# Kernel optimization log

Measured on AMD Instinct MI355X. Metric: run time of the kernel, lower is better.

Reference implementation:

```python
import jax, jax.numpy as jnp
import numpy as np

B, N, E, H, TOP_K = 2, 2048, 1024, 16, 64
Dh = E // H


def _linear_init(k, fan_in, shape):
    bound = 1.0 / np.sqrt(fan_in)
    return jax.random.uniform(k, shape, jnp.float32, -bound, bound)


def setup_inputs() -> dict:
    key = jax.random.key(0)
    ks = jax.random.split(key, 11)
    return {
        "query": jax.random.normal(ks[0], (B, N, E), jnp.float32),
        "key": jax.random.normal(ks[1], (B, N, E), jnp.float32),
        "value": jax.random.normal(ks[2], (B, N, E), jnp.float32),
        "Wq": _linear_init(ks[3], E, (E, E)),
        "bq": _linear_init(ks[4], E, (E,)),
        "Wk": _linear_init(ks[5], E, (E, E)),
        "bk": _linear_init(ks[6], E, (E,)),
        "Wv": _linear_init(ks[7], E, (E, E)),
        "bv": _linear_init(ks[8], E, (E,)),
        "Wo": _linear_init(ks[9], E, (E, E)),
        "bo": _linear_init(ks[10], E, (E,)),
    }


def _split_heads(x):
    # (B, N, E) -> (B*H, N, Dh)
    return x.reshape(B, N, H, Dh).transpose(0, 2, 1, 3).reshape(B * H, N, Dh)


def _merge_heads(x):
    # (B*H, N, Dh) -> (B, N, E)
    return x.reshape(B, H, N, Dh).transpose(0, 2, 1, 3).reshape(B, N, E)


def _topk_attention(q, k, v, top_k):
    # q,k,v: (BH, N, Dh). Faithful to _classical_efficient_attention:
    # scores scaled by sqrt(last dim of Q) == sqrt(Dh).
    scores = jnp.einsum("bqd,bkd->bqk", q, k) / jnp.sqrt(jnp.float32(q.shape[-1]))
    top_scores, top_idx = jax.lax.top_k(scores, min(top_k, scores.shape[-1]))
    w = jax.nn.softmax(top_scores, axis=-1)  # (BH, Nq, K)
    # gather V rows: (BH, 1, Nk, Dh) indexed along axis 2 -> (BH, Nq, K, Dh)
    vals = jnp.take_along_axis(v[:, None, :, :], top_idx[..., None], axis=2)
    return jnp.einsum("bqk,bqkd->bqd", w, vals)


def reference(query, key, value, Wq, bq, Wk, bk, Wv, bv, Wo, bo):
    q = _split_heads(query @ Wq.T + bq)
    k = _split_heads(key @ Wk.T + bk)
    v = _split_heads(value @ Wv.T + bv)
    out = _topk_attention(q, k, v, TOP_K)
    return _merge_heads(out) @ Wo.T + bo
```

## Files before the change

kernel.cpp:

```cpp
#include <hip/hip_runtime.h>
#include <stdint.h>
#include <math.h>

#define Bk 2
#define Nk 2048
#define Ek 1024
#define Hk 16
#define DHk 64
#define BLENDW 5e-5
#define PRECAND 96
#define CANDCAP 128

using short8 = __attribute__((ext_vector_type(8))) short;
using f32x4  = __attribute__((ext_vector_type(4))) float;

__device__ __forceinline__ unsigned short bf16rne(float f) {
    const unsigned u = __float_as_uint(f);
    return (unsigned short)((u + 0x7FFFu + ((u >> 16) & 1u)) >> 16);
}

__global__ __launch_bounds__(256) void cvt_split(
    const float* __restrict__ in, unsigned short* __restrict__ oh,
    unsigned short* __restrict__ ol)
{
    const int i = blockIdx.x * 256 + threadIdx.x;
    const float4 a = ((const float4*)in)[i * 2];
    const float4 b = ((const float4*)in)[i * 2 + 1];
    float x[8] = {a.x, a.y, a.z, a.w, b.x, b.y, b.z, b.w};
    unsigned short hs[8], ls[8];
#pragma unroll
    for (int j = 0; j < 8; ++j) {
        hs[j] = bf16rne(x[j]);
        const float hf = __uint_as_float((unsigned)hs[j] << 16);
        ls[j] = bf16rne(x[j] - hf);
    }
    uint4 ho, lo;
    ho.x = hs[0] | ((unsigned)hs[1] << 16); ho.y = hs[2] | ((unsigned)hs[3] << 16);
    ho.z = hs[4] | ((unsigned)hs[5] << 16); ho.w = hs[6] | ((unsigned)hs[7] << 16);
    lo.x = ls[0] | ((unsigned)ls[1] << 16); lo.y = ls[2] | ((unsigned)ls[3] << 16);
    lo.z = ls[4] | ((unsigned)ls[5] << 16); lo.w = ls[6] | ((unsigned)ls[7] << 16);
    ((uint4*)oh)[i] = ho;
    ((uint4*)ol)[i] = lo;
}

template<int MODE>
__global__ __launch_bounds__(256, 4) void gemm_mfma(
    const unsigned short* __restrict__ Xh, const unsigned short* __restrict__ Xl,
    const unsigned short* __restrict__ Wh, const unsigned short* __restrict__ Wl,
    const float* __restrict__ bias, float* __restrict__ out,
    unsigned short* __restrict__ obf)
{
    __shared__ unsigned short Ah[128][40], Al[128][40];
    __shared__ unsigned short Bh[64][40],  Bl[64][40];

    const int tid  = threadIdx.x;
    const int lane = tid & 63;
    const int wv   = tid >> 6;
    const int n16  = lane & 15;
    const int quad = lane >> 4;
    const int mBase = blockIdx.y * 128;
    const int nBase = blockIdx.x * 64;

    f32x4 acc[2][4];
#pragma unroll
    for (int i = 0; i < 2; ++i)
#pragma unroll
        for (int j = 0; j < 4; ++j) acc[i][j] = (f32x4){0.f, 0.f, 0.f, 0.f};

    const int arow = tid >> 1, aoff = (tid & 1) * 16;
    const int brow = tid >> 2, boff = (tid & 3) * 8;
    const size_t aIdx = (size_t)(mBase + arow) * Ek + aoff;
    const size_t bIdx = (size_t)(nBase + brow) * Ek + boff;

    for (int kt = 0; kt < Ek; kt += 32) {
        const uint4 ah0 = *(const uint4*)(Xh + aIdx + kt);
        const uint4 ah1 = *(const uint4*)(Xh + aIdx + kt + 8);
        const uint4 al0 = *(const uint4*)(Xl + aIdx + kt);
        const uint4 al1 = *(const uint4*)(Xl + aIdx + kt + 8);
        const uint4 bh0 = *(const uint4*)(Wh + bIdx + kt);
        const uint4 bl0 = *(const uint4*)(Wl + bIdx + kt);
        __syncthreads();
        *(uint4*)&Ah[arow][aoff]     = ah0;
        *(uint4*)&Ah[arow][aoff + 8] = ah1;
        *(uint4*)&Al[arow][aoff]     = al0;
        *(uint4*)&Al[arow][aoff + 8] = al1;
        *(uint4*)&Bh[brow][boff]     = bh0;
        *(uint4*)&Bl[brow][boff]     = bl0;
        __syncthreads();

        const short8 fa_h0 = *(const short8*)&Ah[wv*32 +      n16][quad*8];
        const short8 fa_l0 = *(const short8*)&Al[wv*32 +      n16][quad*8];
        const short8 fa_h1 = *(const short8*)&Ah[wv*32 + 16 + n16][quad*8];
        const short8 fa_l1 = *(const short8*)&Al[wv*32 + 16 + n16][quad*8];
#pragma unroll
        for (int ct = 0; ct < 4; ++ct) {
            const short8 fb_h = *(const short8*)&Bh[ct*16 + n16][quad*8];
            const short8 fb_l = *(const short8*)&Bl[ct*16 + n16][quad*8];
            acc[0][ct] = __builtin_amdgcn_mfma_f32_16x16x32_bf16(fa_h0, fb_h, acc[0][ct], 0, 0, 0);
            acc[0][ct] = __builtin_amdgcn_mfma_f32_16x16x32_bf16(fa_h0, fb_l, acc[0][ct], 0, 0, 0);
            acc[0][ct] = __builtin_amdgcn_mfma_f32_16x16x32_bf16(fa_l0, fb_h, acc[0][ct], 0, 0, 0);
            acc[1][ct] = __builtin_amdgcn_mfma_f32_16x16x32_bf16(fa_h1, fb_h, acc[1][ct], 0, 0, 0);
            acc[1][ct] = __builtin_amdgcn_mfma_f32_16x16x32_bf16(fa_h1, fb_l, acc[1][ct], 0, 0, 0);
            acc[1][ct] = __builtin_amdgcn_mfma_f32_16x16x32_bf16(fa_l1, fb_h, acc[1][ct], 0, 0, 0);
        }
    }

#pragma unroll
    for (int mt = 0; mt < 2; ++mt)
#pragma unroll
    for (int ct = 0; ct < 4; ++ct) {
        const int c  = nBase + ct*16 + n16;
        const float bv = bias[c];
#pragma unroll
        for (int reg = 0; reg < 4; ++reg) {
            const int m = mBase + wv*32 + mt*16 + quad*4 + reg;
            const float o = acc[mt][ct][reg] + bv;
            size_t dst;
            if (MODE == 0) {
                dst = (size_t)m * Ek + c;
            } else {
                const int bb = m >> 11, nn = m & 2047;
                const int hh = c >> 6,  dd = c & 63;
                dst = (((size_t)(bb*Hk + hh) * Nk) + nn) * DHk + dd;
            }
            out[dst] = o;
            if (MODE == 1 && obf) obf[dst] = bf16rne(o);
        }
    }
}

__device__ __forceinline__ unsigned fkey(float s) {
    const unsigned b = __float_as_uint(s);
    return (b & 0x80000000u) ? ~b : (b | 0x80000000u);
}
__device__ __forceinline__ unsigned long long dkey(double s) {
    unsigned long long b = (unsigned long long)__double_as_longlong(s);
    return (b & 0x8000000000000000ull) ? ~b : (b | 0x8000000000000000ull);
}
__device__ __forceinline__ double dinv(unsigned long long u) {
    const unsigned long long b =
        (u & 0x8000000000000000ull) ? (u & 0x7fffffffffffffffull) : ~u;
    return __longlong_as_double((long long)b);
}
__device__ __forceinline__ unsigned wave_umin(unsigned v) {
#pragma unroll
    for (int off = 32; off > 0; off >>= 1) {
        const unsigned o = (unsigned)__shfl_xor((int)v, off);
        v = v < o ? v : o;
    }
    return v;
}
__device__ __forceinline__ unsigned wave_umax(unsigned v) {
#pragma unroll
    for (int off = 32; off > 0; off >>= 1) {
        const unsigned o = (unsigned)__shfl_xor((int)v, off);
        v = v > o ? v : o;
    }
    return v;
}
__device__ __forceinline__ int wave_sum_i(int v) {
#pragma unroll
    for (int off = 32; off > 0; off >>= 1) v += __shfl_xor(v, off);
    return v;
}

__device__ __forceinline__ void proc_row(
    const int lane, const int lrow,
    unsigned s0, unsigned s1, unsigned s2, unsigned s3,
    unsigned s4, unsigned s5, unsigned s6, unsigned s7,
    unsigned s8, unsigned s9, unsigned s10, unsigned s11,
    unsigned s12, unsigned s13, unsigned s14, unsigned s15,
    const float* __restrict__ Kb, const float (*qsf)[68],
    unsigned long long (*ck)[CANDCAP], unsigned (*ci)[CANDCAP],
    unsigned (*sel_idx)[64], float (*sel_val)[64], unsigned (*eq_idx)[64],
    int& i65_out, float& lam_out)
{
    const unsigned long long lmask = (1ull << lane) - 1ull;

    const unsigned q0 = s0 << 16,  q1 = s1 << 16,  q2 = s2 << 16,  q3 = s3 << 16;
    const unsigned q4 = s4 << 16,  q5 = s5 << 16,  q6 = s6 << 16,  q7 = s7 << 16;
    const unsigned q8 = s8 << 16,  q9 = s9 << 16,  q10 = s10 << 16, q11 = s11 << 16;
    const unsigned q12 = s12 << 16, q13 = s13 << 16, q14 = s14 << 16, q15 = s15 << 16;

    unsigned m1 = 0u, m2 = 0u;
#define T2(V) { const unsigned t_ = (V) < m1 ? (V) : m1; \
                m1 = m1 > (V) ? m1 : (V);  m2 = m2 > t_ ? m2 : t_; }
    T2(s0)  T2(s1)  T2(s2)  T2(s3)  T2(s4)  T2(s5)  T2(s6)  T2(s7)
    T2(s8)  T2(s9)  T2(s10) T2(s11) T2(s12) T2(s13) T2(s14) T2(s15)
    T2(q0)  T2(q1)  T2(q2)  T2(q3)  T2(q4)  T2(q5)  T2(q6)  T2(q7)
    T2(q8)  T2(q9)  T2(q10) T2(q11) T2(q12) T2(q13) T2(q14) T2(q15)
#undef T2
    unsigned lo16 = wave_umin(m2) >> 16;
    unsigned hi16 = wave_umax(m1) >> 16;

    while (lo16 < hi16) {
        const unsigned mid = lo16 + ((hi16 - lo16) >> 1) + 1u;
        const unsigned M = mid << 16;
        int c0 = 0, c1 = 0, c2 = 0, c3 = 0;
        c0 += (s0  >= M); c0 += (q0  >= M); c0 += (s1  >= M); c0 += (q1  >= M);
        c0 += (s2  >= M); c0 += (q2  >= M); c0 += (s3  >= M); c0 += (q3  >= M);
        c1 += (s4  >= M); c1 += (q4  >= M); c1 += (s5  >= M); c1 += (q5  >= M);
        c1 += (s6  >= M); c1 += (q6  >= M); c1 += (s7  >= M); c1 += (q7  >= M);
        c2 += (s8  >= M); c2 += (q8  >= M); c2 += (s9  >= M); c2 += (q9  >= M);
        c2 += (s10 >= M); c2 += (q10 >= M); c2 += (s11 >= M); c2 += (q11 >= M);
        c3 += (s12 >= M); c3 += (q12 >= M); c3 += (s13 >= M); c3 += (q13 >= M);
        c3 += (s14 >= M); c3 += (q14 >= M); c3 += (s15 >= M); c3 += (q15 >= M);
        int c = wave_sum_i((c0 + c1) + (c2 + c3));
        c = __builtin_amdgcn_readfirstlane(c);
        if (c >= PRECAND) {
            lo16 = mid;
            if (c <= CANDCAP) break;
        } else hi16 = mid - 1u;
    }
    const unsigned THsh = lo16 << 16;

    int nc = 0;
#define COLH(IDX, PRED) { \
        const bool g = (PRED); \
        const unsigned long long m = __ballot(g); \
        if (g) { \
            const int pos = nc + __popcll(m & lmask); \
            if (pos < CANDCAP) \
                ci[lrow][pos] = (unsigned)((((IDX) >> 3) * 512) + (((IDX) & 7) * 64) + lane); \
        } \
        nc += __popcll(m); }
#define COLW(W, S, Q) COLH(2*(W), (Q) >= THsh) COLH(2*(W)+1, (S) >= THsh)
    COLW(0, s0, q0)    COLW(1, s1, q1)    COLW(2, s2, q2)    COLW(3, s3, q3)
    COLW(4, s4, q4)    COLW(5, s5, q5)    COLW(6, s6, q6)    COLW(7, s7, q7)
    COLW(8, s8, q8)    COLW(9, s9, q9)    COLW(10, s10, q10) COLW(11, s11, q11)
    COLW(12, s12, q12) COLW(13, s13, q13) COLW(14, s14, q14) COLW(15, s15, q15)
#undef COLW
#undef COLH
    if (nc > CANDCAP) nc = CANDCAP;

    const int c8 = lane >> 3, d8 = lane & 7;
    const float* qrow = &qsf[lrow][d8 * 8];
    const double qd0 = (double)qrow[0], qd1 = (double)qrow[1];
    const double qd2 = (double)qrow[2], qd3 = (double)qrow[3];
    const double qd4 = (double)qrow[4], qd5 = (double)qrow[5];
    const double qd6 = (double)qrow[6], qd7 = (double)qrow[7];
    const int nb = (nc + 7) >> 3;
    for (int b = 0; b < nb; ++b) {
        const int s  = b * 8 + c8;
        const int s2 = s < nc ? s : nc - 1;
        const unsigned cidx = ci[lrow][s2];
        const unsigned kb32 = (cidx << 6) + (unsigned)(d8 * 8);
        const float2 kv0 = *(const float2*)(Kb + kb32);
        const float2 kv1 = *(const float2*)(Kb + kb32 + 2);
        const float2 kv2 = *(const float2*)(Kb + kb32 + 4);
        const float2 kv3 = *(const float2*)(Kb + kb32 + 6);
        double acc = 0.0;
        acc = fma(qd0, (double)kv0.x, acc);
        acc = fma(qd1, (double)kv0.y, acc);
        acc = fma(qd2, (double)kv1.x, acc);
        acc = fma(qd3, (double)kv1.y, acc);
        acc = fma(qd4, (double)kv2.x, acc);
        acc = fma(qd5, (double)kv2.y, acc);
        acc = fma(qd6, (double)kv3.x, acc);
        acc = fma(qd7, (double)kv3.y, acc);
        acc += __shfl_xor(acc, 1);
        acc += __shfl_xor(acc, 2);
        acc += __shfl_xor(acc, 4);
        if (d8 == 0 && s < nc) ck[lrow][s] = dkey(acc * 0.125);
    }

    const unsigned long long k0 = (lane      < nc) ? ck[lrow][lane]      : 0ull;
    const unsigned long long k1 = (lane + 64 < nc) ? ck[lrow][lane + 64] : 0ull;
    const unsigned idx0 = ci[lrow][lane];
    const unsigned idx1 = ci[lrow][(lane + 64) & (CANDCAP - 1)];
    const unsigned kh0 = (unsigned)(k0 >> 32), kh1 = (unsigned)(k1 >> 32);
    const unsigned kl0 = (unsigned)k0,         kl1 = (unsigned)k1;

    unsigned H;
    {
        const unsigned i0 = (k0 != 0ull) ? kh0 : 0xFFFFFFFFu;
        const unsigned i1 = (k1 != 0ull) ? kh1 : 0xFFFFFFFFu;
        unsigned lo = wave_umin(i0 < i1 ? i0 : i1);
        unsigned hi = wave_umax(kh0 > kh1 ? kh0 : kh1);
        bool done = false;
        while (lo < hi) {
            const unsigned mid = lo + ((hi - lo) >> 1) + 1u;
            const int c = __popcll(__ballot(kh0 >= mid))
                        + __popcll(__ballot(kh1 >= mid));
            if (c == 64) {
                const unsigned v0 = (kh0 >= mid) ? kh0 : 0xFFFFFFFFu;
                const unsigned v1 = (kh1 >= mid) ? kh1 : 0xFFFFFFFFu;
                H = wave_umin(v0 < v1 ? v0 : v1);
                done = true; break;
            }
            if (c >= 64) lo = mid; else hi = mid - 1u;
        }
        if (!done) H = lo;
    }
    const int cGtHi = __popcll(__ballot(kh0 > H))
                    + __popcll(__ballot(kh1 > H));
    const int need1 = 64 - cGtHi;

    const bool e0v = (kh0 == H) && (k0 != 0ull);
    const bool e1v = (kh1 == H) && (k1 != 0ull);
    const int cEq = __popcll(__ballot(e0v)) + __popcll(__ballot(e1v));
    unsigned Tlo;
    if (need1 == cEq) {
        const unsigned v0 = e0v ? kl0 : 0xFFFFFFFFu;
        const unsigned v1 = e1v ? kl1 : 0xFFFFFFFFu;
        Tlo = wave_umin(v0 < v1 ? v0 : v1);
    } else if (need1 == 1) {
        const unsigned v0 = e0v ? kl0 : 0u;
        const unsigned v1 = e1v ? kl1 : 0u;
        Tlo = wave_umax(v0 > v1 ? v0 : v1);
    } else {
        unsigned lo = 0u, hi = 0xFFFFFFFFu;
        bool done = false;
        while (lo < hi) {
            const unsigned mid = lo + ((hi - lo) >> 1) + 1u;
            const int c = __popcll(__ballot(e0v && kl0 >= mid))
                        + __popcll(__ballot(e1v && kl1 >= mid));
            if (c == need1) {
                const unsigned v0 = (e0v && kl0 >= mid) ? kl0 : 0xFFFFFFFFu;
                const unsigned v1 = (e1v && kl1 >= mid) ? kl1 : 0xFFFFFFFFu;
                Tlo = wave_umin(v0 < v1 ? v0 : v1);
                done = true; break;
            }
            if (c >= need1) lo = mid; else hi = mid - 1u;
        }
        if (!done) Tlo = lo;
    }
    const unsigned long long T = ((unsigned long long)H << 32) | Tlo;

    int base = 0;
    {
        const bool g0 = k0 > T;
        unsigned long long m = __ballot(g0);
        if (g0) {
            const int pos = base + __popcll(m & lmask);
            sel_idx[lrow][pos] = idx0; sel_val[lrow][pos] = (float)dinv(k0);
        }
        base += __popcll(m);
        const bool g1 = k1 > T;
        m = __ballot(g1);
        if (g1) {
            const int pos = base + __popcll(m & lmask);
            sel_idx[lrow][pos] = idx1; sel_val[lrow][pos] = (float)dinv(k1);
        }
        base += __popcll(m);
    }

    int ne = 0;
    {
        const bool e0 = k0 == T;
        unsigned long long m = __ballot(e0);
        if (e0) {
            const int pos = ne + __popcll(m & lmask);
            if (pos < 64) eq_idx[lrow][pos] = idx0;
        }
        ne += __popcll(m);
        const bool e1 = k1 == T;
        m = __ballot(e1);
        if (e1) {
            const int pos = ne + __popcll(m & lmask);
            if (pos < 64) eq_idx[lrow][pos] = idx1;
        }
        ne += __popcll(m);
    }
    if (ne > 64) ne = 64;

    const int   need = 64 - base;
    const float tvf  = (float)dinv(T);
    if (lane < need) {
        unsigned my = 0u;
        for (int j = 0; j < ne; ++j) {
            const unsigned v = eq_idx[lrow][j];
            int rank = 0;
            for (int j2 = 0; j2 < ne; ++j2) rank += (eq_idx[lrow][j2] < v) ? 1 : 0;
            if (rank == lane) my = v;
        }
        sel_idx[lrow][base + lane] = my;
        sel_val[lrow][base + lane] = tvf;
    }

    unsigned long long m2k = 0ull;
    if (k0 < T && k0 > m2k) m2k = k0;
    if (k1 < T && k1 > m2k) m2k = k1;
#pragma unroll
    for (int off = 32; off > 0; off >>= 1) {
        const unsigned long long o =
            (unsigned long long)__shfl_xor((long long)m2k, off);
        if (o > m2k) m2k = o;
    }
    int i65 = 0;
    {
        unsigned long long mm = __ballot(k0 == m2k && m2k != 0ull);
        if (mm) i65 = __shfl((int)idx0, (int)(__ffsll((long long)mm) - 1));
        else {
            mm = __ballot(k1 == m2k && m2k != 0ull);
            if (mm) i65 = __shfl((int)idx1, (int)(__ffsll((long long)mm) - 1));
        }
    }
    double fr = (dinv(T) - dinv(m2k)) * (1.0 / BLENDW);
    if (fr > 1.0) fr = 1.0;
    i65_out = i65;
    lam_out = (m2k == 0ull) ? 0.f : (float)(0.5 * (1.0 - fr));
}

__global__ __launch_bounds__(1024, 8) void attn_topk_mfma(
    const float* __restrict__ qf, const float* __restrict__ kf,
    const unsigned short* __restrict__ kbf,
    const float* __restrict__ vh, float* __restrict__ outm)
{
    __shared__ __align__(16) char uS[33024];
    float (*sc)[516] = (float(*)[516])uS;
    unsigned long long (*ck)[CANDCAP] = (unsigned long long(*)[CANDCAP])uS;
    unsigned (*ci)[CANDCAP] = (unsigned(*)[CANDCAP])(uS + 16384);

    __shared__ float          qsf[16][68];
    __shared__ unsigned short qbf[16][72];
    __shared__ unsigned sel_idx[16][64];
    __shared__ float    sel_val[16][64];
    __shared__ unsigned eq_idx[16][64];

    const int tid  = threadIdx.x;
    const int lane = tid & 63;
    const int wv   = tid >> 6;

    const int wid  = (blockIdx.x & 7) * 512 + (blockIdx.x >> 3);
    const int slot = wid >> 7;
    const int qt   = wid & 127;
    const int bb   = slot >> 4;
    const int hh   = slot & 15;

    const float*          Qb = qf  + (size_t)slot * Nk * DHk + (size_t)qt * 16 * DHk;
    const float*          Kb = kf  + (size_t)slot * Nk * DHk;
    const unsigned short* KB = kbf + (size_t)slot * Nk * DHk;
    const float*          Vb = vh  + (size_t)slot * Nk * DHk;

    {
        const int r = tid >> 6, d = tid & 63;
        const float qv = Qb[r * DHk + d];
        qsf[r][d] = qv;
        qbf[r][d] = bf16rne(qv);
    }
    __syncthreads();

    const int n16  = lane & 15;
    const int quad = lane >> 4;
    short8 afrag0, afrag1;
    afrag0 = *(const short8*)&qbf[n16][quad * 8];
    afrag1 = *(const short8*)&qbf[n16][32 + quad * 8];

    unsigned p0, p1, p2, p3, p4, p5, p6, p7;
    unsigned p8, p9, p10, p11, p12, p13, p14, p15;
    const int rowD = quad * 4;

#define QK_TILE(CH, T, ACC) { \
    const unsigned short* kp = KB + ((size_t)(CH) * 512 + (wv * 2 + (T)) * 16 + n16) * DHk + quad * 8; \
    const short8 b0_ = *(const short8*)(kp); \
    const short8 b1_ = *(const short8*)(kp + 32); \
    ACC = __builtin_amdgcn_mfma_f32_16x16x32_bf16(afrag0, b0_, ACC, 0, 0, 0); \
    ACC = __builtin_amdgcn_mfma_f32_16x16x32_bf16(afrag1, b1_, ACC, 0, 0, 0); \
}
#define SC_STORE(T, ACC) { \
    const int ccol = (wv * 2 + (T)) * 16 + n16; \
    sc[rowD + 0][ccol] = ACC[0]; sc[rowD + 1][ccol] = ACC[1]; \
    sc[rowD + 2][ccol] = ACC[2]; sc[rowD + 3][ccol] = ACC[3]; \
}
#define PACKW(J, DEST) { \
    const unsigned lo_ = fkey(sc[wv][(2*(J)    ) * 64 + lane]) >> 16; \
    const unsigned hi_ = fkey(sc[wv][(2*(J) + 1) * 64 + lane]) >> 16; \
    DEST = lo_ | (hi_ << 16); \
}
#define DO_CHUNK(CH, D0, D1, D2, D3) { \
    f32x4 ac0 = {0.f,0.f,0.f,0.f}, ac1 = {0.f,0.f,0.f,0.f}; \
    QK_TILE(CH, 0, ac0) QK_TILE(CH, 1, ac1) \
    __syncthreads();                    \
    SC_STORE(0, ac0) SC_STORE(1, ac1) \
    __syncthreads(); \
    PACKW(0, D0) PACKW(1, D1) PACKW(2, D2) PACKW(3, D3) \
}
    DO_CHUNK(0, p0,  p1,  p2,  p3)
    DO_CHUNK(1, p4,  p5,  p6,  p7)
    DO_CHUNK(2, p8,  p9,  p10, p11)
    DO_CHUNK(3, p12, p13, p14, p15)
#undef DO_CHUNK
#undef PACKW
#undef SC_STORE
#undef QK_TILE

    __syncthreads();

    int i65_0; float lam_0;
    proc_row(lane, wv,
             p0, p1, p2, p3, p4, p5, p6, p7,
             p8, p9, p10, p11, p12, p13, p14, p15,
             Kb, qsf, ck, ci, sel_idx, sel_val, eq_idx, i65_0, lam_0);

    {
        const float    sv = sel_val[wv][lane];
        const unsigned vi = sel_idx[wv][lane];
        float mx = sv;
#pragma unroll
        for (int off = 32; off > 0; off >>= 1)
            mx = fmaxf(mx, __shfl_xor(mx, off));
        float p = __expf(sv - mx);
        float Z = p;
#pragma unroll
        for (int off = 32; off > 0; off >>= 1)
            Z += __shfl_xor(Z, off);
        const float w = p / Z;

        float acc = 0.f;
#pragma unroll 8
        for (int j = 0; j < 64; ++j) {
            const float wj = __shfl(w, j);
            const int   ij = __shfl((int)vi, j);
            const unsigned voff = ((unsigned)ij << 6) + (unsigned)lane;
            acc = fmaf(wj, Vb[voff], acc);
        }
        {
            const float wT  = __shfl(w, 63);
            const int   i64 = __shfl((int)vi, 63);
            const unsigned o65 = ((unsigned)i65_0 << 6) + (unsigned)lane;
            const unsigned o64 = ((unsigned)i64   << 6) + (unsigned)lane;
            acc += wT * lam_0 * (Vb[o65] - Vb[o64]);
        }
        const int gq = qt * 16 + wv;
        outm[((size_t)bb * Nk + gq) * Ek + hh * DHk + lane] = acc;
    }
}

extern "C" void kernel_launch(void* const* d_in, const int* in_sizes, int n_in,
                              void* d_out, int out_size, void* d_ws, size_t ws_size,
                              hipStream_t stream)
{
    const float* query = (const float*)d_in[0];
    const float* key   = (const float*)d_in[1];
    const float* value = (const float*)d_in[2];
    const float* Wq    = (const float*)d_in[3];
    const float* bq    = (const float*)d_in[4];
    const float* Wk    = (const float*)d_in[5];
    const float* bk    = (const float*)d_in[6];
    const float* Wv    = (const float*)d_in[7];
    const float* bv    = (const float*)d_in[8];
    const float* Wo    = (const float*)d_in[9];
    const float* bo    = (const float*)d_in[10];
    float* out = (float*)d_out;
    (void)in_sizes; (void)n_in; (void)out_size; (void)ws_size;

    const size_t seg  = (size_t)(Bk * Hk) * Nk * DHk;
    const size_t wseg = (size_t)Ek * Ek;
    float* qfp = (float*)d_ws;
    float* kfp = qfp + seg;
    float* vws = kfp + seg;
    float* aws = vws + seg;
    unsigned short* kbf = (unsigned short*)(aws + seg);
    unsigned short* xh  = kbf + seg;
    unsigned short* xl  = xh + seg;
    unsigned short* wh  = xl + seg;
    unsigned short* wl  = wh + wseg;

    const dim3 blk(256);
    const dim3 gG(16, 32);
    const int  gX = (int)(seg  / 2048);
    const int  gW = (int)(wseg / 2048);

    hipLaunchKernelGGL(cvt_split, dim3(gX), blk, 0, stream, query, xh, xl);
    hipLaunchKernelGGL(cvt_split, dim3(gW), blk, 0, stream, Wq, wh, wl);
    hipLaunchKernelGGL((gemm_mfma<1>), gG, blk, 0, stream, xh, xl, wh, wl, bq, qfp, (unsigned short*)nullptr);
    hipLaunchKernelGGL(cvt_split, dim3(gX), blk, 0, stream, key, xh, xl);
    hipLaunchKernelGGL(cvt_split, dim3(gW), blk, 0, stream, Wk, wh, wl);
    hipLaunchKernelGGL((gemm_mfma<1>), gG, blk, 0, stream, xh, xl, wh, wl, bk, kfp, kbf);
    hipLaunchKernelGGL(cvt_split, dim3(gX), blk, 0, stream, value, xh, xl);
    hipLaunchKernelGGL(cvt_split, dim3(gW), blk, 0, stream, Wv, wh, wl);
    hipLaunchKernelGGL((gemm_mfma<1>), gG, blk, 0, stream, xh, xl, wh, wl, bv, vws, (unsigned short*)nullptr);
    hipLaunchKernelGGL(attn_topk_mfma, dim3(32 * 128), dim3(1024), 0, stream,
                       qfp, kfp, kbf, vws, aws);
    hipLaunchKernelGGL(cvt_split, dim3(gX), blk, 0, stream, aws, xh, xl);
    hipLaunchKernelGGL(cvt_split, dim3(gW), blk, 0, stream, Wo, wh, wl);
    hipLaunchKernelGGL((gemm_mfma<0>), gG, blk, 0, stream, xh, xl, wh, wl, bo, out, (unsigned short*)nullptr);
}
```

Before: 645.7 us.

## Use 512-thread GEMM tiles, DPP wave reductions, and packed LDS weight/index pairs

```diff
diff --git a/kernel.cpp b/kernel.cpp
--- a/kernel.cpp
+++ b/kernel.cpp
@@ -44,7 +44,7 @@
 }
 
 template<int MODE>
-__global__ __launch_bounds__(256, 4) void gemm_mfma(
+__global__ __launch_bounds__(512, 4) void gemm_mfma(
     const unsigned short* __restrict__ Xh, const unsigned short* __restrict__ Xl,
     const unsigned short* __restrict__ Wh, const unsigned short* __restrict__ Wl,
     const float* __restrict__ bias, float* __restrict__ out,
@@ -61,60 +61,47 @@
     const int mBase = blockIdx.y * 128;
     const int nBase = blockIdx.x * 64;
 
-    f32x4 acc[2][4];
-#pragma unroll
-    for (int i = 0; i < 2; ++i)
-#pragma unroll
-        for (int j = 0; j < 4; ++j) acc[i][j] = (f32x4){0.f, 0.f, 0.f, 0.f};
-
-    const int arow = tid >> 1, aoff = (tid & 1) * 16;
-    const int brow = tid >> 2, boff = (tid & 3) * 8;
+    f32x4 acc[4];
+#pragma unroll
+    for (int j = 0; j < 4; ++j) acc[j] = (f32x4){0.f, 0.f, 0.f, 0.f};
+
+    const int arow = tid >> 2, aoff = (tid & 3) * 8;
+    const int brow = tid >> 3, boff = (tid & 7) * 4;
     const size_t aIdx = (size_t)(mBase + arow) * Ek + aoff;
     const size_t bIdx = (size_t)(nBase + brow) * Ek + boff;
 
     for (int kt = 0; kt < Ek; kt += 32) {
         const uint4 ah0 = *(const uint4*)(Xh + aIdx + kt);
-        const uint4 ah1 = *(const uint4*)(Xh + aIdx + kt + 8);
         const uint4 al0 = *(const uint4*)(Xl + aIdx + kt);
-        const uint4 al1 = *(const uint4*)(Xl + aIdx + kt + 8);
-        const uint4 bh0 = *(const uint4*)(Wh + bIdx + kt);
-        const uint4 bl0 = *(const uint4*)(Wl + bIdx + kt);
+        const uint2 bh0 = *(const uint2*)(Wh + bIdx + kt);
+        const uint2 bl0 = *(const uint2*)(Wl + bIdx + kt);
         __syncthreads();
-        *(uint4*)&Ah[arow][aoff]     = ah0;
-        *(uint4*)&Ah[arow][aoff + 8] = ah1;
-        *(uint4*)&Al[arow][aoff]     = al0;
-        *(uint4*)&Al[arow][aoff + 8] = al1;
-        *(uint4*)&Bh[brow][boff]     = bh0;
-        *(uint4*)&Bl[brow][boff]     = bl0;
+        *(uint4*)&Ah[arow][aoff] = ah0;
+        *(uint4*)&Al[arow][aoff] = al0;
+        *(uint2*)&Bh[brow][boff] = bh0;
+        *(uint2*)&Bl[brow][boff] = bl0;
         __syncthreads();
 
-        const short8 fa_h0 = *(const short8*)&Ah[wv*32 +      n16][quad*8];
-        const short8 fa_l0 = *(const short8*)&Al[wv*32 +      n16][quad*8];
-        const short8 fa_h1 = *(const short8*)&Ah[wv*32 + 16 + n16][quad*8];
-        const short8 fa_l1 = *(const short8*)&Al[wv*32 + 16 + n16][quad*8];
+        const short8 fa_h = *(const short8*)&Ah[wv*16 + n16][quad*8];
+        const short8 fa_l = *(const short8*)&Al[wv*16 + n16][quad*8];
 #pragma unroll
         for (int ct = 0; ct < 4; ++ct) {
             const short8 fb_h = *(const short8*)&Bh[ct*16 + n16][quad*8];
             const short8 fb_l = *(const short8*)&Bl[ct*16 + n16][quad*8];
-            acc[0][ct] = __builtin_amdgcn_mfma_f32_16x16x32_bf16(fa_h0, fb_h, acc[0][ct], 0, 0, 0);
-            acc[0][ct] = __builtin_amdgcn_mfma_f32_16x16x32_bf16(fa_h0, fb_l, acc[0][ct], 0, 0, 0);
-            acc[0][ct] = __builtin_amdgcn_mfma_f32_16x16x32_bf16(fa_l0, fb_h, acc[0][ct], 0, 0, 0);
-            acc[1][ct] = __builtin_amdgcn_mfma_f32_16x16x32_bf16(fa_h1, fb_h, acc[1][ct], 0, 0, 0);
-            acc[1][ct] = __builtin_amdgcn_mfma_f32_16x16x32_bf16(fa_h1, fb_l, acc[1][ct], 0, 0, 0);
-            acc[1][ct] = __builtin_amdgcn_mfma_f32_16x16x32_bf16(fa_l1, fb_h, acc[1][ct], 0, 0, 0);
-        }
-    }
-
-#pragma unroll
-    for (int mt = 0; mt < 2; ++mt)
+            acc[ct] = __builtin_amdgcn_mfma_f32_16x16x32_bf16(fa_h, fb_h, acc[ct], 0, 0, 0);
+            acc[ct] = __builtin_amdgcn_mfma_f32_16x16x32_bf16(fa_h, fb_l, acc[ct], 0, 0, 0);
+            acc[ct] = __builtin_amdgcn_mfma_f32_16x16x32_bf16(fa_l, fb_h, acc[ct], 0, 0, 0);
+        }
+    }
+
 #pragma unroll
     for (int ct = 0; ct < 4; ++ct) {
         const int c  = nBase + ct*16 + n16;
         const float bv = bias[c];
 #pragma unroll
         for (int reg = 0; reg < 4; ++reg) {
-            const int m = mBase + wv*32 + mt*16 + quad*4 + reg;
-            const float o = acc[mt][ct][reg] + bv;
+            const int m = mBase + wv*16 + quad*4 + reg;
+            const float o = acc[ct][reg] + bv;
             size_t dst;
             if (MODE == 0) {
                 dst = (size_t)m * Ek + c;
@@ -142,26 +129,40 @@
         (u & 0x8000000000000000ull) ? (u & 0x7fffffffffffffffull) : ~u;
     return __longlong_as_double((long long)b);
 }
-__device__ __forceinline__ unsigned wave_umin(unsigned v) {
-#pragma unroll
-    for (int off = 32; off > 0; off >>= 1) {
-        const unsigned o = (unsigned)__shfl_xor((int)v, off);
-        v = v < o ? v : o;
-    }
-    return v;
-}
-__device__ __forceinline__ unsigned wave_umax(unsigned v) {
-#pragma unroll
-    for (int off = 32; off > 0; off >>= 1) {
-        const unsigned o = (unsigned)__shfl_xor((int)v, off);
-        v = v > o ? v : o;
-    }
-    return v;
-}
-__device__ __forceinline__ int wave_sum_i(int v) {
-#pragma unroll
-    for (int off = 32; off > 0; off >>= 1) v += __shfl_xor(v, off);
-    return v;
+
+__device__ __forceinline__ int dpp_wsum_i32(int x) {
+#define STEP(C) x += __builtin_amdgcn_update_dpp(0, x, C, 0xf, 0xf, true);
+    STEP(0x111) STEP(0x112) STEP(0x114) STEP(0x118) STEP(0x142) STEP(0x143)
+#undef STEP
+    return __builtin_amdgcn_readlane(x, 63);
+}
+__device__ __forceinline__ float dpp_wsum_f32(float x) {
+#define STEP(C) { const int t_ = __builtin_amdgcn_update_dpp(0, __float_as_int(x), C, 0xf, 0xf, true); \
+                  x += __int_as_float(t_); }
+    STEP(0x111) STEP(0x112) STEP(0x114) STEP(0x118) STEP(0x142) STEP(0x143)
+#undef STEP
+    return __int_as_float(__builtin_amdgcn_readlane(__float_as_int(x), 63));
+}
+__device__ __forceinline__ float dpp_wmax_f32(float x) {
+#define STEP(C) { const int t_ = __builtin_amdgcn_update_dpp(__float_as_int(x), __float_as_int(x), C, 0xf, 0xf, false); \
+                  x = fmaxf(x, __int_as_float(t_)); }
+    STEP(0x111) STEP(0x112) STEP(0x114) STEP(0x118) STEP(0x142) STEP(0x143)
+#undef STEP
+    return __int_as_float(__builtin_amdgcn_readlane(__float_as_int(x), 63));
+}
+__device__ __forceinline__ unsigned dpp_wmin_u32(unsigned x) {
+#define STEP(C) { const unsigned t_ = (unsigned)__builtin_amdgcn_update_dpp((int)x, (int)x, C, 0xf, 0xf, false); \
+                  x = x < t_ ? x : t_; }
+    STEP(0x111) STEP(0x112) STEP(0x114) STEP(0x118) STEP(0x142) STEP(0x143)
+#undef STEP
+    return (unsigned)__builtin_amdgcn_readlane((int)x, 63);
+}
+__device__ __forceinline__ unsigned dpp_wmax_u32(unsigned x) {
+#define STEP(C) { const unsigned t_ = (unsigned)__builtin_amdgcn_update_dpp((int)x, (int)x, C, 0xf, 0xf, false); \
+                  x = x > t_ ? x : t_; }
+    STEP(0x111) STEP(0x112) STEP(0x114) STEP(0x118) STEP(0x142) STEP(0x143)
+#undef STEP
+    return (unsigned)__builtin_amdgcn_readlane((int)x, 63);
 }
 
 __device__ __forceinline__ void proc_row(
@@ -172,7 +173,7 @@
     unsigned s12, unsigned s13, unsigned s14, unsigned s15,
     const float* __restrict__ Kb, const float (*qsf)[68],
     unsigned long long (*ck)[CANDCAP], unsigned (*ci)[CANDCAP],
-    unsigned (*sel_idx)[64], float (*sel_val)[64], unsigned (*eq_idx)[64],
+    unsigned long long (*wvi)[64], unsigned (*eq_idx)[64],
     int& i65_out, float& lam_out)
 {
     const unsigned long long lmask = (1ull << lane) - 1ull;
@@ -190,8 +191,8 @@
     T2(q0)  T2(q1)  T2(q2)  T2(q3)  T2(q4)  T2(q5)  T2(q6)  T2(q7)
     T2(q8)  T2(q9)  T2(q10) T2(q11) T2(q12) T2(q13) T2(q14) T2(q15)
 #undef T2
-    unsigned lo16 = wave_umin(m2) >> 16;
-    unsigned hi16 = wave_umax(m1) >> 16;
+    unsigned lo16 = dpp_wmin_u32(m2) >> 16;
+    unsigned hi16 = dpp_wmax_u32(m1) >> 16;
 
     while (lo16 < hi16) {
         const unsigned mid = lo16 + ((hi16 - lo16) >> 1) + 1u;
@@ -205,8 +206,7 @@
         c2 += (s10 >= M); c2 += (q10 >= M); c2 += (s11 >= M); c2 += (q11 >= M);
         c3 += (s12 >= M); c3 += (q12 >= M); c3 += (s13 >= M); c3 += (q13 >= M);
         c3 += (s14 >= M); c3 += (q14 >= M); c3 += (s15 >= M); c3 += (q15 >= M);
-        int c = wave_sum_i((c0 + c1) + (c2 + c3));
-        c = __builtin_amdgcn_readfirstlane(c);
+        const int c = dpp_wsum_i32((c0 + c1) + (c2 + c3));
         if (c >= PRECAND) {
             lo16 = mid;
             if (c <= CANDCAP) break;
@@ -275,8 +275,8 @@
     {
         const unsigned i0 = (k0 != 0ull) ? kh0 : 0xFFFFFFFFu;
         const unsigned i1 = (k1 != 0ull) ? kh1 : 0xFFFFFFFFu;
-        unsigned lo = wave_umin(i0 < i1 ? i0 : i1);
-        unsigned hi = wave_umax(kh0 > kh1 ? kh0 : kh1);
+        unsigned lo = dpp_wmin_u32(i0 < i1 ? i0 : i1);
+        unsigned hi = dpp_wmax_u32(kh0 > kh1 ? kh0 : kh1);
         bool done = false;
         while (lo < hi) {
             const unsigned mid = lo + ((hi - lo) >> 1) + 1u;
@@ -285,7 +285,7 @@
             if (c == 64) {
                 const unsigned v0 = (kh0 >= mid) ? kh0 : 0xFFFFFFFFu;
                 const unsigned v1 = (kh1 >= mid) ? kh1 : 0xFFFFFFFFu;
-                H = wave_umin(v0 < v1 ? v0 : v1);
+                H = dpp_wmin_u32(v0 < v1 ? v0 : v1);
                 done = true; break;
             }
             if (c >= 64) lo = mid; else hi = mid - 1u;
@@ -303,11 +303,11 @@
     if (need1 == cEq) {
         const unsigned v0 = e0v ? kl0 : 0xFFFFFFFFu;
         const unsigned v1 = e1v ? kl1 : 0xFFFFFFFFu;
-        Tlo = wave_umin(v0 < v1 ? v0 : v1);
+        Tlo = dpp_wmin_u32(v0 < v1 ? v0 : v1);
     } else if (need1 == 1) {
         const unsigned v0 = e0v ? kl0 : 0u;
         const unsigned v1 = e1v ? kl1 : 0u;
-        Tlo = wave_umax(v0 > v1 ? v0 : v1);
+        Tlo = dpp_wmax_u32(v0 > v1 ? v0 : v1);
     } else {
         unsigned lo = 0u, hi = 0xFFFFFFFFu;
         bool done = false;
@@ -318,7 +318,7 @@
             if (c == need1) {
                 const unsigned v0 = (e0v && kl0 >= mid) ? kl0 : 0xFFFFFFFFu;
                 const unsigned v1 = (e1v && kl1 >= mid) ? kl1 : 0xFFFFFFFFu;
-                Tlo = wave_umin(v0 < v1 ? v0 : v1);
+                Tlo = dpp_wmin_u32(v0 < v1 ? v0 : v1);
                 done = true; break;
             }
             if (c >= need1) lo = mid; else hi = mid - 1u;
@@ -333,14 +333,16 @@
         unsigned long long m = __ballot(g0);
         if (g0) {
             const int pos = base + __popcll(m & lmask);
-            sel_idx[lrow][pos] = idx0; sel_val[lrow][pos] = (float)dinv(k0);
+            wvi[lrow][pos] = ((unsigned long long)__float_as_uint((float)dinv(k0)) << 32)
+                           | (unsigned long long)idx0;
         }
         base += __popcll(m);
         const bool g1 = k1 > T;
         m = __ballot(g1);
         if (g1) {
             const int pos = base + __popcll(m & lmask);
-            sel_idx[lrow][pos] = idx1; sel_val[lrow][pos] = (float)dinv(k1);
+            wvi[lrow][pos] = ((unsigned long long)__float_as_uint((float)dinv(k1)) << 32)
+                           | (unsigned long long)idx1;
         }
         base += __popcll(m);
     }
@@ -374,8 +376,8 @@
             for (int j2 = 0; j2 < ne; ++j2) rank += (eq_idx[lrow][j2] < v) ? 1 : 0;
             if (rank == lane) my = v;
         }
-        sel_idx[lrow][base + lane] = my;
-        sel_val[lrow][base + lane] = tvf;
+        wvi[lrow][base + lane] = ((unsigned long long)__float_as_uint(tvf) << 32)
+                               | (unsigned long long)my;
     }
 
     unsigned long long m2k = 0ull;
@@ -414,8 +416,7 @@
 
     __shared__ float          qsf[16][68];
     __shared__ unsigned short qbf[16][72];
-    __shared__ unsigned sel_idx[16][64];
-    __shared__ float    sel_val[16][64];
+    __shared__ unsigned long long wvi[16][64];
     __shared__ unsigned eq_idx[16][64];
 
     const int tid  = threadIdx.x;
@@ -491,36 +492,34 @@
     proc_row(lane, wv,
              p0, p1, p2, p3, p4, p5, p6, p7,
              p8, p9, p10, p11, p12, p13, p14, p15,
-             Kb, qsf, ck, ci, sel_idx, sel_val, eq_idx, i65_0, lam_0);
+             Kb, qsf, ck, ci, wvi, eq_idx, i65_0, lam_0);
 
     {
-        const float    sv = sel_val[wv][lane];
-        const unsigned vi = sel_idx[wv][lane];
-        float mx = sv;
-#pragma unroll
-        for (int off = 32; off > 0; off >>= 1)
-            mx = fmaxf(mx, __shfl_xor(mx, off));
-        float p = __expf(sv - mx);
-        float Z = p;
-#pragma unroll
-        for (int off = 32; off > 0; off >>= 1)
-            Z += __shfl_xor(Z, off);
-        const float w = p / Z;
+        const unsigned long long e = wvi[wv][lane];
+        const float    sv = __uint_as_float((unsigned)(e >> 32));
+        const unsigned vi = (unsigned)e;
+        const float mx = dpp_wmax_f32(sv);
+        const float p  = __expf(sv - mx);
+        const float Z  = dpp_wsum_f32(p);
+        const float w  = p / Z;
+        wvi[wv][lane] = ((unsigned long long)__float_as_uint(w) << 32)
+                      | (unsigned long long)vi;
 
         float acc = 0.f;
-#pragma unroll 8
+#pragma unroll
         for (int j = 0; j < 64; ++j) {
-            const float wj = __shfl(w, j);
-            const int   ij = __shfl((int)vi, j);
-            const unsigned voff = ((unsigned)ij << 6) + (unsigned)lane;
-            acc = fmaf(wj, Vb[voff], acc);
+            const unsigned long long ej = wvi[wv][j];
+            const float wj = __uint_as_float((unsigned)(ej >> 32));
+            const unsigned ij = (unsigned)ej;
+            acc = fmaf(wj, Vb[(ij << 6) + (unsigned)lane], acc);
         }
         {
-            const float wT  = __shfl(w, 63);
-            const int   i64 = __shfl((int)vi, 63);
-            const unsigned o65 = ((unsigned)i65_0 << 6) + (unsigned)lane;
-            const unsigned o64 = ((unsigned)i64   << 6) + (unsigned)lane;
-            acc += wT * lam_0 * (Vb[o65] - Vb[o64]);
+            const unsigned long long e63 = wvi[wv][63];
+            const float    wT  = __uint_as_float((unsigned)(e63 >> 32));
+            const unsigned i64 = (unsigned)e63;
+            acc += wT * lam_0 *
+                   (Vb[((unsigned)i65_0 << 6) + (unsigned)lane]
+                  - Vb[(i64 << 6) + (unsigned)lane]);
         }
         const int gq = qt * 16 + wv;
         outm[((size_t)bb * Nk + gq) * Ek + hh * DHk + lane] = acc;
@@ -558,22 +557,23 @@
     unsigned short* wl  = wh + wseg;
 
     const dim3 blk(256);
+    const dim3 blkG(512);
     const dim3 gG(16, 32);
     const int  gX = (int)(seg  / 2048);
     const int  gW = (int)(wseg / 2048);
 
     hipLaunchKernelGGL(cvt_split, dim3(gX), blk, 0, stream, query, xh, xl);
     hipLaunchKernelGGL(cvt_split, dim3(gW), blk, 0, stream, Wq, wh, wl);
-    hipLaunchKernelGGL((gemm_mfma<1>), gG, blk, 0, stream, xh, xl, wh, wl, bq, qfp, (unsigned short*)nullptr);
+    hipLaunchKernelGGL((gemm_mfma<1>), gG, blkG, 0, stream, xh, xl, wh, wl, bq, qfp, (unsigned short*)nullptr);
     hipLaunchKernelGGL(cvt_split, dim3(gX), blk, 0, stream, key, xh, xl);
     hipLaunchKernelGGL(cvt_split, dim3(gW), blk, 0, stream, Wk, wh, wl);
-    hipLaunchKernelGGL((gemm_mfma<1>), gG, blk, 0, stream, xh, xl, wh, wl, bk, kfp, kbf);
+    hipLaunchKernelGGL((gemm_mfma<1>), gG, blkG, 0, stream, xh, xl, wh, wl, bk, kfp, kbf);
     hipLaunchKernelGGL(cvt_split, dim3(gX), blk, 0, stream, value, xh, xl);
     hipLaunchKernelGGL(cvt_split, dim3(gW), blk, 0, stream, Wv, wh, wl);
-    hipLaunchKernelGGL((gemm_mfma<1>), gG, blk, 0, stream, xh, xl, wh, wl, bv, vws, (unsigned short*)nullptr);
+    hipLaunchKernelGGL((gemm_mfma<1>), gG, blkG, 0, stream, xh, xl, wh, wl, bv, vws, (unsigned short*)nullptr);
     hipLaunchKernelGGL(attn_topk_mfma, dim3(32 * 128), dim3(1024), 0, stream,
                        qfp, kfp, kbf, vws, aws);
     hipLaunchKernelGGL(cvt_split, dim3(gX), blk, 0, stream, aws, xh, xl);
     hipLaunchKernelGGL(cvt_split, dim3(gW), blk, 0, stream, Wo, wh, wl);
-    hipLaunchKernelGGL((gemm_mfma<0>), gG, blk, 0, stream, xh, xl, wh, wl, bo, out, (unsigned short*)nullptr);
-}
+    hipLaunchKernelGGL((gemm_mfma<0>), gG, blkG, 0, stream, xh, xl, wh, wl, bo, out, (unsigned short*)nullptr);
+}
```

Result: faster. 601.3 us (-6.9%).
